# Performance work log

Measured on AMD Instinct MI355X. Metric: run time of the kernel, lower is better.

## Reference

```python
import jax, jax.numpy as jnp
import numpy as np

N = 20000   # nodes
E = 320000  # edges (before self loops)
IN = 128    # in_channel
H = 8       # heads
C = 128     # out_channels per head
HC = H * C  # 1024
G = 64      # graphs in batch


def _w(k, shape):
    s = 1.0 / np.sqrt(shape[-1])
    return jax.random.uniform(k, shape, jnp.float32, -s, s)


def setup_inputs() -> dict:
    key = jax.random.key(0)
    ks = jax.random.split(key, 12)
    return {
        "x": jax.random.normal(ks[0], (N, IN), jnp.float32),
        "edge_index": jax.random.randint(ks[1], (2, E), 0, N, dtype=jnp.int64),
        "batch": jnp.sort(jax.random.randint(ks[2], (N,), 0, G, dtype=jnp.int64)),
        # GATv2Conv params
        "Wl": _w(ks[3], (HC, IN)), "bl": jnp.zeros((HC,), jnp.float32),
        "Wr": _w(ks[4], (HC, IN)), "br": jnp.zeros((HC,), jnp.float32),
        "att": _w(ks[5], (H, C)),
        "Wres": _w(ks[6], (HC, IN)),
        "bias_conv": jnp.zeros((HC,), jnp.float32),
        # post-attention Linear(HC -> C)
        "Wlin": _w(ks[7], (C, HC)), "blin": jnp.zeros((C,), jnp.float32),
        # MLP head 128 -> 16 -> 32 -> 5
        "W1": _w(ks[8], (16, C)), "b1": jnp.zeros((16,), jnp.float32),
        "W2": _w(ks[9], (32, 16)), "b2": jnp.zeros((32,), jnp.float32),
        "W3": _w(ks[10], (5, 32)), "b3": jnp.zeros((5,), jnp.float32),
    }


def reference(x, edge_index, batch, Wl, bl, Wr, br, att, Wres, bias_conv,
              Wlin, blin, W1, b1, W2, b2, W3, b3):
    # --- GATv2Conv (PyG semantics: add_self_loops=True, concat=True, residual) ---
    loops = jnp.arange(N)
    src = jnp.concatenate([edge_index[0], loops])  # [E+N]
    dst = jnp.concatenate([edge_index[1], loops])
    x_l = (x @ Wl.T + bl).reshape(N, H, C)
    x_r = (x @ Wr.T + br).reshape(N, H, C)
    # per-edge attention logits
    e = jax.nn.leaky_relu(x_l[src] + x_r[dst], 0.2)        # [E+N, H, C]
    logits = jnp.einsum('ehc,hc->eh', e, att)              # [E+N, H]
    # segment softmax over destination neighborhoods
    m = jax.ops.segment_max(logits, dst, num_segments=N)
    a = jnp.exp(logits - m[dst])
    denom = jax.ops.segment_sum(a, dst, num_segments=N)
    alpha = a / (denom[dst] + 1e-16)                       # [E+N, H]
    # scatter-add weighted messages
    out = jax.ops.segment_sum(x_l[src] * alpha[:, :, None], dst,
                              num_segments=N).reshape(N, HC)
    out = out + x @ Wres.T + bias_conv                     # residual + bias
    # --- Linear + ELU ---
    h = jax.nn.elu(out @ Wlin.T + blin)                    # [N, C]
    # --- global mean pool per graph ---
    cnt = jax.ops.segment_sum(jnp.ones((N,), h.dtype), batch, num_segments=G)
    pooled = jax.ops.segment_sum(h, batch, num_segments=G) / jnp.maximum(cnt, 1.0)[:, None]
    # --- MLP head ---
    y = jax.nn.relu(pooled @ W1.T + b1)
    y = jax.nn.relu(y @ W2.T + b2)
    return y @ W3.T + b3                                   # [G, 5]
```

## Files before the change

### kernel.cpp

```cpp
#include <hip/hip_runtime.h>
#include <hip/hip_bf16.h>
#include <math.h>

#define N_NODES 20000
#define N_EDGES 320000
#define IN_CH   128
#define HEADS   8
#define CPH     128
#define HCH     1024
#define NG      64
#define ETOT    (N_EDGES + N_NODES)
#define NCVT    768
#define NROWT   157
#define GRID_P  (NROWT * 16)

typedef __attribute__((ext_vector_type(8))) short s8v;
typedef __attribute__((ext_vector_type(4))) float f4v;
typedef __attribute__((ext_vector_type(8))) float f8v;
typedef __attribute__((ext_vector_type(4))) unsigned short u16x4;
typedef __attribute__((ext_vector_type(8))) unsigned short u16x8;

__device__ __forceinline__ unsigned short bf16_rne(float f) {
    unsigned u = __float_as_uint(f);
    unsigned r = u + 0x7fffu + ((u >> 16) & 1u);
    return (unsigned short)(r >> 16);
}
__device__ __forceinline__ float bf16_to_f(unsigned short h) {
    return __uint_as_float((unsigned)h << 16);
}

__global__ void init_kernel(int* __restrict__ deg, float* __restrict__ pooled) {
    int i = blockIdx.x * blockDim.x + threadIdx.x;
    if (i < N_NODES) deg[i] = 0;
    if (i < NG * CPH) pooled[i] = 0.0f;
}

__global__ void cvt_all(const float* __restrict__ x,  const float* __restrict__ Wl,
                        const float* __restrict__ Wr, const float* __restrict__ Wlin,
                        unsigned short* __restrict__ xhi,  unsigned short* __restrict__ xlo,
                        unsigned short* __restrict__ wlhi, unsigned short* __restrict__ wllo,
                        unsigned short* __restrict__ wrhi, unsigned short* __restrict__ wrlo,
                        unsigned short* __restrict__ wnhi, unsigned short* __restrict__ wnlo,
                        const int* __restrict__ ei, int* __restrict__ deg,
                        const float* __restrict__ Wres, const float* __restrict__ bias_conv,
                        const float* __restrict__ blin,
                        unsigned short* __restrict__ wchi, unsigned short* __restrict__ wclo,
                        float* __restrict__ bcomb)
{
    const int t = threadIdx.x;
    if (blockIdx.x < NCVT) {
        const int NX = N_NODES * IN_CH, NW = HCH * IN_CH;
        const int TOT4 = (NX + 3 * NW) >> 2;
        const int stride = NCVT * 256;
        for (int q = blockIdx.x * 256 + t; q < TOT4; q += stride) {
            int i = q << 2;
            const float* s; unsigned short *hi, *lo; int k;
            if (i < NX)               { s = x;    hi = xhi;  lo = xlo;  k = i; }
            else if (i < NX + NW)     { s = Wl;   hi = wlhi; lo = wllo; k = i - NX; }
            else if (i < NX + 2 * NW) { s = Wr;   hi = wrhi; lo = wrlo; k = i - NX - NW; }
            else                      { s = Wlin; hi = wnhi; lo = wnlo; k = i - NX - 2 * NW; }
            f4v f = *(const f4v*)&s[k];
            u16x4 h, l;
            #pragma unroll
            for (int e = 0; e < 4; ++e) {
                unsigned short hh = bf16_rne(f[e]);
                h[e] = hh;
                l[e] = bf16_rne(f[e] - bf16_to_f(hh));
            }
            *(u16x4*)&hi[k] = h;
            *(u16x4*)&lo[k] = l;
        }
        for (int e = blockIdx.x * 256 + t; e < ETOT; e += stride) {
            int dst = (e < N_EDGES) ? ei[N_EDGES + e] : (e - N_EDGES);
            atomicAdd(&deg[dst], 1);
        }
    } else if (t < 128) {
        const int j = blockIdx.x - NCVT;
        float s = 0.0f, pb = 0.0f;
        for (int m = 0; m < HCH; ++m) {
            float wl = Wlin[j * HCH + m];
            s  += wl * Wres[m * IN_CH + t];
            pb += wl * bias_conv[m];
        }
        unsigned short h = bf16_rne(s);
        wchi[j * IN_CH + t] = h;
        wclo[j * IN_CH + t] = bf16_rne(s - bf16_to_f(h));
        if (t == 0) bcomb[j] = blin[j] + pb;
    }
}

__global__ __launch_bounds__(256) void proj_gemm(
    const unsigned short* __restrict__ Ahi, const unsigned short* __restrict__ Alo,
    const unsigned short* __restrict__ WLhi, const unsigned short* __restrict__ WLlo,
    const unsigned short* __restrict__ WRhi, const unsigned short* __restrict__ WRlo,
    const float* __restrict__ bl, const float* __restrict__ br,
    const float* __restrict__ att,
    unsigned short* __restrict__ xl_h, unsigned short* __restrict__ xr_h,
    float* __restrict__ dl, float* __restrict__ dr, int M)
{
    __shared__ unsigned short cst[128][136];
    const int id  = blockIdx.x;
    const int nat = (id & 7) * (GRID_P / 8) + (id >> 3);
    const int bx  = nat >> 4;
    const int by  = nat & 15;
    const int t    = threadIdx.x;
    const int wave = t >> 6, lane = t & 63;
    const int wr = wave >> 1, wc = wave & 1;
    const int l15 = lane & 15, lg = lane >> 4;
    const int m0 = bx * 128 + wr * 64;
    const int sel = by >> 3;
    const int hh  = by & 7;
    const int col0 = hh * 128;
    const unsigned short* Whi = sel ? WRhi : WLhi;
    const unsigned short* Wlo = sel ? WRlo : WLlo;
    const float* bias = sel ? br : bl;
    unsigned short* C = sel ? xr_h : xl_h;
    float* D = sel ? dr : dl;
    const int koff = lg * 8;
    const int K = IN_CH;

    int rowA[4], colB[4];
    #pragma unroll
    for (int i = 0; i < 4; ++i) { int r = m0 + i * 16 + l15; rowA[i] = r < M ? r : M - 1; }
    #pragma unroll
    for (int j = 0; j < 4; ++j) colB[j] = col0 + wc * 64 + j * 16 + l15;

    float bj[4];
    #pragma unroll
    for (int j = 0; j < 4; ++j) bj[j] = bias[colB[j]];

    f4v acc[4][4];
    #pragma unroll
    for (int i = 0; i < 4; ++i)
        #pragma unroll
        for (int j = 0; j < 4; ++j) acc[i][j] = (f4v){0.f, 0.f, 0.f, 0.f};

    for (int k0 = 0; k0 < K; k0 += 32) {
        s8v ah[4], al[4], bh[4], blv[4];
        #pragma unroll
        for (int i = 0; i < 4; ++i) {
            size_t off = (size_t)rowA[i] * K + k0 + koff;
            ah[i] = *(const s8v*)&Ahi[off];
            al[i] = *(const s8v*)&Alo[off];
        }
        #pragma unroll
        for (int j = 0; j < 4; ++j) {
            size_t off = (size_t)colB[j] * K + k0 + koff;
            bh[j]  = *(const s8v*)&Whi[off];
            blv[j] = *(const s8v*)&Wlo[off];
        }
        #pragma unroll
        for (int i = 0; i < 4; ++i)
            #pragma unroll
            for (int j = 0; j < 4; ++j) {
                acc[i][j] = __builtin_amdgcn_mfma_f32_16x16x32_bf16(ah[i], bh[j],  acc[i][j], 0, 0, 0);
                acc[i][j] = __builtin_amdgcn_mfma_f32_16x16x32_bf16(ah[i], blv[j], acc[i][j], 0, 0, 0);
                acc[i][j] = __builtin_amdgcn_mfma_f32_16x16x32_bf16(al[i], bh[j],  acc[i][j], 0, 0, 0);
            }
    }

    #pragma unroll
    for (int i = 0; i < 4; ++i)
        #pragma unroll
        for (int r = 0; r < 4; ++r) {
            int lr = wr * 64 + i * 16 + lg * 4 + r;
            #pragma unroll
            for (int j = 0; j < 4; ++j)
                cst[lr][wc * 64 + j * 16 + l15] = bf16_rne(acc[i][j][r] + bj[j]);
        }
    __syncthreads();

    {
        const int c8  = (t & 15) * 8;
        const int r16 = t >> 4;
        #pragma unroll
        for (int it = 0; it < 8; ++it) {
            int lr = it * 16 + r16;
            int row = bx * 128 + lr;
            if (row >= M) continue;
            u16x8 v = *(const u16x8*)&cst[lr][c8];
            *(u16x8*)&C[(size_t)row * HCH + col0 + c8] = v;
        }
    }

    {
        const int r2  = t >> 1;
        const int ch0 = (t & 1) * 64;
        float q = 0.0f;
        #pragma unroll
        for (int c = 0; c < 64; c += 8) {
            u16x8 cv = *(const u16x8*)&cst[r2][ch0 + c];
            f4v a0 = *(const f4v*)&att[hh * 128 + ch0 + c];
            f4v a1 = *(const f4v*)&att[hh * 128 + ch0 + c + 4];
            q = fmaf(a0[0], bf16_to_f(cv[0]), q);
            q = fmaf(a0[1], bf16_to_f(cv[1]), q);
            q = fmaf(a0[2], bf16_to_f(cv[2]), q);
            q = fmaf(a0[3], bf16_to_f(cv[3]), q);
            q = fmaf(a1[0], bf16_to_f(cv[4]), q);
            q = fmaf(a1[1], bf16_to_f(cv[5]), q);
            q = fmaf(a1[2], bf16_to_f(cv[6]), q);
            q = fmaf(a1[3], bf16_to_f(cv[7]), q);
        }
        q += __shfl_xor(q, 1, 64);
        int row = bx * 128 + r2;
        if ((t & 1) == 0 && row < M) D[row * 8 + hh] = q;
    }
}

__global__ __launch_bounds__(128) void mfma_gemm2(
    const unsigned short* __restrict__ A1h,
    const unsigned short* __restrict__ B1hi, const unsigned short* __restrict__ B1lo, int K1,
    const unsigned short* __restrict__ A2hi, const unsigned short* __restrict__ A2lo,
    const unsigned short* __restrict__ B2hi, const unsigned short* __restrict__ B2lo, int K2,
    const float* __restrict__ bias, const int* __restrict__ batch,
    float* __restrict__ pooled, int M)
{
    __shared__ float cst[64][130];
    __shared__ int batch_s[64];
    const int t    = threadIdx.x;
    const int wc   = t >> 6, lane = t & 63;
    const int l15 = lane & 15, lg = lane >> 4;
    const int m0 = blockIdx.x * 64;
    const int n0 = wc * 64;
    const int koff = lg * 8;

    if (t < 64) {
        int row = m0 + t;
        batch_s[t] = (row < M) ? batch[row] : -1;
    }

    int rowA[4], colB[4];
    #pragma unroll
    for (int i = 0; i < 4; ++i) { int r = m0 + i * 16 + l15; rowA[i] = r < M ? r : M - 1; }
    #pragma unroll
    for (int j = 0; j < 4; ++j) colB[j] = n0 + j * 16 + l15;

    float bj[4];
    #pragma unroll
    for (int j = 0; j < 4; ++j) bj[j] = bias[colB[j]];

    f4v acc[4][4];
    #pragma unroll
    for (int i = 0; i < 4; ++i)
        #pragma unroll
        for (int j = 0; j < 4; ++j) acc[i][j] = (f4v){0.f, 0.f, 0.f, 0.f};

    for (int k0 = 0; k0 < K1; k0 += 32) {
        s8v ah[4], bh[4], blv[4];
        #pragma unroll
        for (int i = 0; i < 4; ++i)
            ah[i] = *(const s8v*)&A1h[(size_t)rowA[i] * K1 + k0 + koff];
        #pragma unroll
        for (int j = 0; j < 4; ++j) {
            size_t off = (size_t)colB[j] * K1 + k0 + koff;
            bh[j]  = *(const s8v*)&B1hi[off];
            blv[j] = *(const s8v*)&B1lo[off];
        }
        #pragma unroll
        for (int i = 0; i < 4; ++i)
            #pragma unroll
            for (int j = 0; j < 4; ++j) {
                acc[i][j] = __builtin_amdgcn_mfma_f32_16x16x32_bf16(ah[i], bh[j],  acc[i][j], 0, 0, 0);
                acc[i][j] = __builtin_amdgcn_mfma_f32_16x16x32_bf16(ah[i], blv[j], acc[i][j], 0, 0, 0);
            }
    }
    for (int k0 = 0; k0 < K2; k0 += 32) {
        s8v ah[4], al[4], bh[4], blv[4];
        #pragma unroll
        for (int i = 0; i < 4; ++i) {
            size_t off = (size_t)rowA[i] * K2 + k0 + koff;
            ah[i] = *(const s8v*)&A2hi[off];
            al[i] = *(const s8v*)&A2lo[off];
        }
        #pragma unroll
        for (int j = 0; j < 4; ++j) {
            size_t off = (size_t)colB[j] * K2 + k0 + koff;
            bh[j]  = *(const s8v*)&B2hi[off];
            blv[j] = *(const s8v*)&B2lo[off];
        }
        #pragma unroll
        for (int i = 0; i < 4; ++i)
            #pragma unroll
            for (int j = 0; j < 4; ++j) {
                acc[i][j] = __builtin_amdgcn_mfma_f32_16x16x32_bf16(ah[i], bh[j],  acc[i][j], 0, 0, 0);
                acc[i][j] = __builtin_amdgcn_mfma_f32_16x16x32_bf16(ah[i], blv[j], acc[i][j], 0, 0, 0);
                acc[i][j] = __builtin_amdgcn_mfma_f32_16x16x32_bf16(al[i], bh[j],  acc[i][j], 0, 0, 0);
            }
    }

    #pragma unroll
    for (int i = 0; i < 4; ++i)
        #pragma unroll
        for (int r = 0; r < 4; ++r) {
            int lr = i * 16 + lg * 4 + r;
            #pragma unroll
            for (int j = 0; j < 4; ++j) {
                float v = acc[i][j][r] + bj[j];
                v = v > 0.0f ? v : expm1f(v);
                cst[lr][n0 + j * 16 + l15] = v;
            }
        }
    __syncthreads();

    const int col = t;
    float run = 0.0f;
    int cur_g = -2;
    #pragma unroll 4
    for (int r = 0; r < 64; ++r) {
        int g = batch_s[r];
        if (g != cur_g) {
            if (cur_g >= 0) atomicAdd(&pooled[cur_g * CPH + col], run);
            run = 0.0f; cur_g = g;
        }
        if (g >= 0) run += cst[r][col];
    }
    if (cur_g >= 0) atomicAdd(&pooled[cur_g * CPH + col], run);
}

__global__ __launch_bounds__(256) void scan_kernel(
    const int* __restrict__ deg, int* __restrict__ rowptr, int* __restrict__ wof)
{
    __shared__ int wsum[4];
    __shared__ int carry_s;
    const int t = threadIdx.x, wave = t >> 6, lane = t & 63;
    if (t == 0) { carry_s = 0; rowptr[0] = 0; }
    __syncthreads();
    for (int base = 0; base < N_NODES; base += 1024) {
        int idx = base + t * 4;
        int d[4], p[4];
        #pragma unroll
        for (int k = 0; k < 4; ++k)
            d[k] = (idx + k < N_NODES) ? deg[idx + k] : 0;
        p[0] = d[0]; p[1] = p[0] + d[1]; p[2] = p[1] + d[2]; p[3] = p[2] + d[3];
        int v = p[3];
        #pragma unroll
        for (int off = 1; off < 64; off <<= 1) {
            int u = __shfl_up(v, off, 64);
            if (lane >= off) v += u;
        }
        if (lane == 63) wsum[wave] = v;
        __syncthreads();
        int woff = carry_s;
        #pragma unroll
        for (int w = 0; w < 4; ++w) if (w < wave) woff += wsum[w];
        int tbase = woff + v - p[3];
        #pragma unroll
        for (int k = 0; k < 4; ++k) {
            if (idx + k < N_NODES) {
                rowptr[idx + k + 1] = tbase + p[k];
                wof[idx + k] = tbase + p[k] - d[k];
            }
        }
        __syncthreads();
        if (t == 255) carry_s = woff + v;
        __syncthreads();
    }
}

__global__ void scatter_kernel(const int* __restrict__ ei, int* __restrict__ wof,
                               int* __restrict__ csr_src)
{
    for (int e = blockIdx.x * blockDim.x + threadIdx.x; e < ETOT;
         e += gridDim.x * blockDim.x) {
        int src, dst;
        if (e < N_EDGES) { src = ei[e]; dst = ei[N_EDGES + e]; }
        else             { src = dst = e - N_EDGES; }
        int p = atomicAdd(&wof[dst], 1);
        csr_src[p] = src;
    }
}

__global__ __launch_bounds__(256) void agg_fused(
    const unsigned short* __restrict__ xl_h, const unsigned short* __restrict__ xr_h,
    const float* __restrict__ att,
    const float* __restrict__ dl, const float* __restrict__ dr,
    const int* __restrict__ rowptr, const int* __restrict__ csr_src,
    unsigned short* __restrict__ agg_h, int dst0)
{
    __shared__ float lds_m[128], lds_s[128];
    __shared__ float lds_acc[8][128];
    const int dst = blockIdx.x + dst0;
    const int t = threadIdx.x;
    const int grp = t >> 7;
    const int u = t & 127;
    const int h = u >> 4;
    const int beg = rowptr[dst], end = rowptr[dst + 1];

    const u16x8 bh8 = *(const u16x8*)&xr_h[(size_t)dst * HCH + u * 8];
    f8v b;
    #pragma unroll
    for (int e = 0; e < 8; ++e) b[e] = bf16_to_f(bh8[e]);
    f8v w04;
    {
        f4v a0 = *(const f4v*)&att[u * 8];
        f4v a1 = *(const f4v*)&att[u * 8 + 4];
        #pragma unroll
        for (int e = 0; e < 4; ++e) { w04[e] = 0.4f * a0[e]; w04[e + 4] = 0.4f * a1[e]; }
    }
    const float pb = 0.6f * dr[dst * 8 + h];

    float m = -__builtin_inff(), s = 0.0f;
    f8v acc = {0.f, 0.f, 0.f, 0.f, 0.f, 0.f, 0.f, 0.f};

    int j = beg + grp * 2;
    for (; j + 1 < end; j += 4) {
        const int s0 = csr_src[j], s1 = csr_src[j + 1];
        const u16x8 vh0 = *(const u16x8*)&xl_h[(size_t)s0 * HCH + u * 8];
        const u16x8 vh1 = *(const u16x8*)&xl_h[(size_t)s1 * HCH + u * 8];
        const float d0 = dl[s0 * 8 + h], d1 = dl[s1 * 8 + h];
        f8v v0, v1;
        #pragma unroll
        for (int e = 0; e < 8; ++e) { v0[e] = bf16_to_f(vh0[e]); v1[e] = bf16_to_f(vh1[e]); }

        float q0 = w04[0] * __builtin_fabsf(v0[0] + b[0]);
        float q1 = w04[0] * __builtin_fabsf(v1[0] + b[0]);
        #pragma unroll
        for (int e = 1; e < 8; ++e) {
            q0 = fmaf(w04[e], __builtin_fabsf(v0[e] + b[e]), q0);
            q1 = fmaf(w04[e], __builtin_fabsf(v1[e] + b[e]), q1);
        }
        #pragma unroll
        for (int off = 8; off; off >>= 1) {
            q0 += __shfl_xor(q0, off, 16);
            q1 += __shfl_xor(q1, off, 16);
        }
        const float p0 = fmaf(0.6f, d0, q0) + pb;
        const float p1 = fmaf(0.6f, d1, q1) + pb;

        const float mx = fmaxf(p0, p1);
        if (mx > m) {
            float scale = __expf(m - mx);
            float e0 = __expf(p0 - mx), e1 = __expf(p1 - mx);
            s = s * scale + e0 + e1;
            acc = acc * scale + v0 * e0 + v1 * e1;
            m = mx;
        } else {
            float e0 = __expf(p0 - m), e1 = __expf(p1 - m);
            s += e0 + e1;
            acc += v0 * e0 + v1 * e1;
        }
    }
    if (j < end) {
        const int s0 = csr_src[j];
        const u16x8 vh0 = *(const u16x8*)&xl_h[(size_t)s0 * HCH + u * 8];
        const float d0 = dl[s0 * 8 + h];
        f8v v0;
        #pragma unroll
        for (int e = 0; e < 8; ++e) v0[e] = bf16_to_f(vh0[e]);
        float q0 = w04[0] * __builtin_fabsf(v0[0] + b[0]);
        #pragma unroll
        for (int e = 1; e < 8; ++e)
            q0 = fmaf(w04[e], __builtin_fabsf(v0[e] + b[e]), q0);
        #pragma unroll
        for (int off = 8; off; off >>= 1) q0 += __shfl_xor(q0, off, 16);
        const float p0 = fmaf(0.6f, d0, q0) + pb;
        if (p0 > m) {
            float scale = __expf(m - p0);
            s = s * scale + 1.0f;
            acc = acc * scale + v0;
            m = p0;
        } else {
            float e0 = __expf(p0 - m);
            s += e0;
            acc += v0 * e0;
        }
    }

    if (grp == 1) {
        lds_m[u] = m;
        lds_s[u] = s;
        #pragma unroll
        for (int e = 0; e < 8; ++e) lds_acc[e][u] = acc[e];
    }
    __syncthreads();
    if (grp == 0) {
        const float m1 = lds_m[u], s1 = lds_s[u];
        const float M  = fmaxf(m, m1);
        const float c0 = __expf(m - M);
        const float c1 = __expf(m1 - M);
        const float S  = s * c0 + s1 * c1;
        const float inv = 1.0f / (S + 1e-16f);
        u16x8 hv;
        #pragma unroll
        for (int e = 0; e < 8; ++e) {
            float r = (acc[e] * c0 + lds_acc[e][u] * c1) * inv;
            hv[e] = bf16_rne(r);
        }
        *(u16x8*)&agg_h[(size_t)dst * HCH + u * 8] = hv;
    }
}

__global__ __launch_bounds__(64) void head_kernel(
    const float* __restrict__ pooled, const int* __restrict__ batch,
    const float* __restrict__ W1, const float* __restrict__ b1,
    const float* __restrict__ W2, const float* __restrict__ b2,
    const float* __restrict__ W3, const float* __restrict__ b3,
    float* __restrict__ out)
{
    const int g = threadIdx.x;
    int lo = 0, hi = N_NODES;
    while (lo < hi) { int mid = (lo + hi) >> 1; if (batch[mid] <  g) lo = mid + 1; else hi = mid; }
    const int s0 = lo;
    hi = N_NODES;
    while (lo < hi) { int mid = (lo + hi) >> 1; if (batch[mid] <= g) lo = mid + 1; else hi = mid; }
    const float inv = 1.0f / fmaxf((float)(lo - s0), 1.0f);

    float y1[16];
    for (int j = 0; j < 16; ++j) {
        float s = b1[j];
        for (int k = 0; k < CPH; ++k) s += W1[j * CPH + k] * (pooled[g * CPH + k] * inv);
        y1[j] = fmaxf(s, 0.0f);
    }
    float y2[32];
    for (int j = 0; j < 32; ++j) {
        float s = b2[j];
        for (int k = 0; k < 16; ++k) s += W2[j * 16 + k] * y1[k];
        y2[j] = fmaxf(s, 0.0f);
    }
    for (int u = 0; u < 5; ++u) {
        float s = b3[u];
        for (int k = 0; k < 32; ++k) s += W3[u * 32 + k] * y2[k];
        out[g * 5 + u] = s;
    }
}

extern "C" void kernel_launch(void* const* d_in, const int* in_sizes, int n_in,
                              void* d_out, int out_size, void* d_ws, size_t ws_size,
                              hipStream_t stream)
{
    const float* x         = (const float*)d_in[0];
    const int*   ei        = (const int*)  d_in[1];
    const int*   batch     = (const int*)  d_in[2];
    const float* Wl        = (const float*)d_in[3];
    const float* bl        = (const float*)d_in[4];
    const float* Wr        = (const float*)d_in[5];
    const float* br        = (const float*)d_in[6];
    const float* att       = (const float*)d_in[7];
    const float* Wres      = (const float*)d_in[8];
    const float* bias_conv = (const float*)d_in[9];
    const float* Wlin      = (const float*)d_in[10];
    const float* blin      = (const float*)d_in[11];
    const float* W1        = (const float*)d_in[12];
    const float* b1        = (const float*)d_in[13];
    const float* W2        = (const float*)d_in[14];
    const float* b2        = (const float*)d_in[15];
    const float* W3        = (const float*)d_in[16];
    const float* b3        = (const float*)d_in[17];
    float* out = (float*)d_out;

    unsigned short* xl_h  = (unsigned short*)d_ws;
    unsigned short* xr_h  = xl_h + (size_t)N_NODES * HCH;
    unsigned short* agg_h = xr_h + (size_t)N_NODES * HCH;
    float* pooled = (float*)(agg_h + (size_t)N_NODES * HCH);
    float* bcomb  = pooled + NG * CPH;
    float* dl     = bcomb + 128;
    float* dr     = dl + (size_t)N_NODES * 8;
    unsigned short* x_hi  = (unsigned short*)(dr + (size_t)N_NODES * 8);
    unsigned short* x_lo  = x_hi  + (size_t)N_NODES * IN_CH;
    unsigned short* wl_hi = x_lo  + (size_t)N_NODES * IN_CH;
    unsigned short* wl_lo = wl_hi + HCH * IN_CH;
    unsigned short* wr_hi = wl_lo + HCH * IN_CH;
    unsigned short* wr_lo = wr_hi + HCH * IN_CH;
    unsigned short* wn_hi = wr_lo + HCH * IN_CH;
    unsigned short* wn_lo = wn_hi + CPH * HCH;
    unsigned short* wc_hi = wn_lo + CPH * HCH;
    unsigned short* wc_lo = wc_hi + CPH * IN_CH;
    int* deg     = (int*)(wc_lo + CPH * IN_CH);
    int* rowptr  = deg + N_NODES;
    int* wof     = rowptr + N_NODES + 1;
    int* csr_src = wof + N_NODES;

    init_kernel<<<(N_NODES + 255) / 256, 256, 0, stream>>>(deg, pooled);

    cvt_all<<<NCVT + 128, 256, 0, stream>>>(x, Wl, Wr, Wlin,
                                            x_hi, x_lo, wl_hi, wl_lo,
                                            wr_hi, wr_lo, wn_hi, wn_lo,
                                            ei, deg,
                                            Wres, bias_conv, blin,
                                            wc_hi, wc_lo, bcomb);

    proj_gemm<<<GRID_P, 256, 0, stream>>>(x_hi, x_lo, wl_hi, wl_lo, wr_hi, wr_lo,
                                          bl, br, att, xl_h, xr_h, dl, dr, N_NODES);

    scan_kernel<<<1, 256, 0, stream>>>(deg, rowptr, wof);
    scatter_kernel<<<1024, 256, 0, stream>>>(ei, wof, csr_src);

    agg_fused<<<N_NODES / 2, 256, 0, stream>>>(xl_h, xr_h, att, dl, dr,
                                               rowptr, csr_src, agg_h, 0);
    agg_fused<<<N_NODES / 2, 256, 0, stream>>>(xl_h, xr_h, att, dl, dr,
                                               rowptr, csr_src, agg_h, N_NODES / 2);

    dim3 g2((N_NODES + 63) / 64, 1);
    mfma_gemm2<<<g2, 128, 0, stream>>>(agg_h, wn_hi, wn_lo, HCH,
                                       x_hi, x_lo, wc_hi, wc_lo, IN_CH,
                                       bcomb, batch, pooled, N_NODES);

    head_kernel<<<1, 64, 0, stream>>>(pooled, batch, W1, b1, W2, b2, W3, b3, out);
}
```

Measured before the change: 430.6 us.

## Store projections head-major and drop low-part A term in projection GEMM

The projected node features xl/xr and the per-head attention dot terms are now stored head-major ([head][node][128]) instead of node-major, and the aggregation kernel indexes that layout. The projection GEMM also drops the x_lo correction term, cutting one MFMA in three and the matching A-low loads. The layout change is meant to make per-head gathers in aggregation land in one contiguous plane per head. Dropping the x low part lowers precision of the split-bf16 emulated fp32 GEMM.

```diff
diff --git a/kernel.cpp b/kernel.cpp
--- a/kernel.cpp
+++ b/kernel.cpp
@@ -13,6 +13,7 @@
 #define NCVT    768
 #define NROWT   157
 #define GRID_P  (NROWT * 16)
+#define PL      ((size_t)N_NODES * 128)
 
 typedef __attribute__((ext_vector_type(8))) short s8v;
 typedef __attribute__((ext_vector_type(4))) float f4v;
@@ -90,7 +91,7 @@
 }
 
 __global__ __launch_bounds__(256) void proj_gemm(
-    const unsigned short* __restrict__ Ahi, const unsigned short* __restrict__ Alo,
+    const unsigned short* __restrict__ Ahi,
     const unsigned short* __restrict__ WLhi, const unsigned short* __restrict__ WLlo,
     const unsigned short* __restrict__ WRhi, const unsigned short* __restrict__ WRlo,
     const float* __restrict__ bl, const float* __restrict__ br,
@@ -136,13 +137,10 @@
         for (int j = 0; j < 4; ++j) acc[i][j] = (f4v){0.f, 0.f, 0.f, 0.f};
 
     for (int k0 = 0; k0 < K; k0 += 32) {
-        s8v ah[4], al[4], bh[4], blv[4];
-        #pragma unroll
-        for (int i = 0; i < 4; ++i) {
-            size_t off = (size_t)rowA[i] * K + k0 + koff;
-            ah[i] = *(const s8v*)&Ahi[off];
-            al[i] = *(const s8v*)&Alo[off];
-        }
+        s8v ah[4], bh[4], blv[4];
+        #pragma unroll
+        for (int i = 0; i < 4; ++i)
+            ah[i] = *(const s8v*)&Ahi[(size_t)rowA[i] * K + k0 + koff];
         #pragma unroll
         for (int j = 0; j < 4; ++j) {
             size_t off = (size_t)colB[j] * K + k0 + koff;
@@ -155,7 +153,6 @@
             for (int j = 0; j < 4; ++j) {
                 acc[i][j] = __builtin_amdgcn_mfma_f32_16x16x32_bf16(ah[i], bh[j],  acc[i][j], 0, 0, 0);
                 acc[i][j] = __builtin_amdgcn_mfma_f32_16x16x32_bf16(ah[i], blv[j], acc[i][j], 0, 0, 0);
-                acc[i][j] = __builtin_amdgcn_mfma_f32_16x16x32_bf16(al[i], bh[j],  acc[i][j], 0, 0, 0);
             }
     }
 
@@ -179,7 +176,7 @@
             int row = bx * 128 + lr;
             if (row >= M) continue;
             u16x8 v = *(const u16x8*)&cst[lr][c8];
-            *(u16x8*)&C[(size_t)row * HCH + col0 + c8] = v;
+            *(u16x8*)&C[(size_t)hh * PL + (size_t)row * 128 + c8] = v;
         }
     }
 
@@ -203,7 +200,7 @@
         }
         q += __shfl_xor(q, 1, 64);
         int row = bx * 128 + r2;
-        if ((t & 1) == 0 && row < M) D[row * 8 + hh] = q;
+        if ((t & 1) == 0 && row < M) D[hh * N_NODES + row] = q;
     }
 }
 
@@ -384,9 +381,11 @@
     const int grp = t >> 7;
     const int u = t & 127;
     const int h = u >> 4;
+    const int c16 = (u & 15) * 8;
+    const size_t pbase = (size_t)h * PL + c16;
     const int beg = rowptr[dst], end = rowptr[dst + 1];
 
-    const u16x8 bh8 = *(const u16x8*)&xr_h[(size_t)dst * HCH + u * 8];
+    const u16x8 bh8 = *(const u16x8*)&xr_h[pbase + (size_t)dst * 128];
     f8v b;
     #pragma unroll
     for (int e = 0; e < 8; ++e) b[e] = bf16_to_f(bh8[e]);
@@ -397,7 +396,7 @@
         #pragma unroll
         for (int e = 0; e < 4; ++e) { w04[e] = 0.4f * a0[e]; w04[e + 4] = 0.4f * a1[e]; }
     }
-    const float pb = 0.6f * dr[dst * 8 + h];
+    const float pb = 0.6f * dr[h * N_NODES + dst];
 
     float m = -__builtin_inff(), s = 0.0f;
     f8v acc = {0.f, 0.f, 0.f, 0.f, 0.f, 0.f, 0.f, 0.f};
@@ -405,9 +404,9 @@
     int j = beg + grp * 2;
     for (; j + 1 < end; j += 4) {
         const int s0 = csr_src[j], s1 = csr_src[j + 1];
-        const u16x8 vh0 = *(const u16x8*)&xl_h[(size_t)s0 * HCH + u * 8];
-        const u16x8 vh1 = *(const u16x8*)&xl_h[(size_t)s1 * HCH + u * 8];
-        const float d0 = dl[s0 * 8 + h], d1 = dl[s1 * 8 + h];
+        const u16x8 vh0 = *(const u16x8*)&xl_h[pbase + (size_t)s0 * 128];
+        const u16x8 vh1 = *(const u16x8*)&xl_h[pbase + (size_t)s1 * 128];
+        const float d0 = dl[h * N_NODES + s0], d1 = dl[h * N_NODES + s1];
         f8v v0, v1;
         #pragma unroll
         for (int e = 0; e < 8; ++e) { v0[e] = bf16_to_f(vh0[e]); v1[e] = bf16_to_f(vh1[e]); }
@@ -442,8 +441,8 @@
     }
     if (j < end) {
         const int s0 = csr_src[j];
-        const u16x8 vh0 = *(const u16x8*)&xl_h[(size_t)s0 * HCH + u * 8];
-        const float d0 = dl[s0 * 8 + h];
+        const u16x8 vh0 = *(const u16x8*)&xl_h[pbase + (size_t)s0 * 128];
+        const float d0 = dl[h * N_NODES + s0];
         f8v v0;
         #pragma unroll
         for (int e = 0; e < 8; ++e) v0[e] = bf16_to_f(vh0[e]);
@@ -579,7 +578,7 @@
                                             Wres, bias_conv, blin,
                                             wc_hi, wc_lo, bcomb);
 
-    proj_gemm<<<GRID_P, 256, 0, stream>>>(x_hi, x_lo, wl_hi, wl_lo, wr_hi, wr_lo,
+    proj_gemm<<<GRID_P, 256, 0, stream>>>(x_hi, wl_hi, wl_lo, wr_hi, wr_lo,
                                           bl, br, att, xl_h, xr_h, dl, dr, N_NODES);
 
     scan_kernel<<<1, 256, 0, stream>>>(deg, rowptr, wof);
```

Result: no change. 423.1 us (-1.8%).
